# Optimization experiments

Hardware: AMD Instinct MI355X
Metric: run time of the kernel (lower is better)

## Reference

```python
import jax, jax.numpy as jnp
import numpy as np

N_NODES = 50000
N_EDGES = 800000
IN_DIM = 128
HID = 32
HEADS = 4
EMB = 64
NEG_SLOPE = 0.2
LN_EPS = 1e-5


def setup_inputs() -> dict:
    key = jax.random.key(0)
    ks = jax.random.split(key, 16)
    s = 0.1
    inp = {
        'x': jax.random.normal(ks[0], (N_NODES, IN_DIM), dtype=jnp.float32),
        'edge_index': jax.random.randint(ks[1], (2, N_EDGES), 0, N_NODES, dtype=jnp.int64),
        # GATConv 1: in=128 -> heads=4, out_per_head=32, concat -> 128
        'W1': jax.random.normal(ks[2], (IN_DIM, HEADS * HID), dtype=jnp.float32) * s,
        'att_src1': jax.random.normal(ks[3], (HEADS, HID), dtype=jnp.float32) * s,
        'att_dst1': jax.random.normal(ks[4], (HEADS, HID), dtype=jnp.float32) * s,
        'b1': jnp.zeros((HEADS * HID,), dtype=jnp.float32),
        'gamma1': jnp.ones((HEADS * HID,), dtype=jnp.float32),
        'beta1': jnp.zeros((HEADS * HID,), dtype=jnp.float32),
        # GATConv 2: in=128 -> heads=1, out=64, concat=False
        'W2': jax.random.normal(ks[5], (HEADS * HID, EMB), dtype=jnp.float32) * s,
        'att_src2': jax.random.normal(ks[6], (1, EMB), dtype=jnp.float32) * s,
        'att_dst2': jax.random.normal(ks[7], (1, EMB), dtype=jnp.float32) * s,
        'b2': jnp.zeros((EMB,), dtype=jnp.float32),
        'gamma2': jnp.ones((EMB,), dtype=jnp.float32),
        'beta2': jnp.zeros((EMB,), dtype=jnp.float32),
    }
    return inp


def _gat_conv(x, src, dst, W, att_src, att_dst):
    # x: [N, F_in]; src/dst: [E'] (self loops included); W: [F_in, H*C]
    N = x.shape[0]
    H, C = att_src.shape
    h = (x @ W).reshape(N, H, C)                          # [N, H, C]
    a_s = jnp.sum(h * att_src, axis=-1)                   # [N, H]
    a_d = jnp.sum(h * att_dst, axis=-1)                   # [N, H]
    e = jax.nn.leaky_relu(a_s[src] + a_d[dst], NEG_SLOPE) # [E', H]
    # segment softmax over destination-node neighborhoods
    m = jax.ops.segment_max(e, dst, num_segments=N)       # [N, H]
    ex = jnp.exp(e - m[dst])
    den = jax.ops.segment_sum(ex, dst, num_segments=N)    # [N, H]
    alpha = ex / den[dst]                                  # [E', H]
    msg = h[src] * alpha[:, :, None]                       # [E', H, C]
    return jax.ops.segment_sum(msg, dst, num_segments=N)  # [N, H, C]


def _layer_norm(x, gamma, beta):
    mu = jnp.mean(x, axis=-1, keepdims=True)
    var = jnp.var(x, axis=-1, keepdims=True)
    return (x - mu) * jax.lax.rsqrt(var + LN_EPS) * gamma + beta


def reference(x, edge_index, W1, att_src1, att_dst1, b1, gamma1, beta1,
              W2, att_src2, att_dst2, b2, gamma2, beta2):
    N = x.shape[0]
    loops = jnp.arange(N, dtype=edge_index.dtype)
    src = jnp.concatenate([edge_index[0], loops])  # PyG add_self_loops=True
    dst = jnp.concatenate([edge_index[1], loops])

    # gat1: heads=4, concat=True
    h1 = _gat_conv(x, src, dst, W1, att_src1, att_dst1)   # [N, 4, 32]
    h1 = h1.reshape(N, -1) + b1                            # [N, 128]
    h1 = jax.nn.relu(_layer_norm(h1, gamma1, beta1))
    # dropout is identity in eval mode

    # gat2: heads=1, concat=False (mean over the single head)
    h2 = _gat_conv(h1, src, dst, W2, att_src2, att_dst2)  # [N, 1, 64]
    h2 = h2.mean(axis=1) + b2                              # [N, 64]
    return _layer_norm(h2, gamma2, beta2)
```

## Files before the change

kernel.cpp:

```cpp
#include <hip/hip_runtime.h>
#include <hip/hip_bf16.h>
#include <math.h>

#define N_NODES 50000
#define N_EDGES 800000
#define HEADS 4
#define HID 32
#define D1 128
#define D2 64
#define NEG_SLOPE 0.2f
#define LN_EPS 1e-5f

#define NB_SCAN ((N_NODES + 255) / 256)
#define CAP 64
#define GB1 (((N_NODES + 127) / 128) * 2)
#define DEGB 784

__device__ __forceinline__ float lrelu(float x) { return x > 0.f ? x : NEG_SLOPE * x; }
__device__ __forceinline__ float bf2f(__hip_bfloat16 v) { return __bfloat162float(v); }

__global__ __launch_bounds__(256) void gemm1_att1_degree_kernel(
    const float* __restrict__ X, const float* __restrict__ W,
    __hip_bfloat16* __restrict__ Y,
    const float* __restrict__ att_src, const float* __restrict__ att_dst,
    float* __restrict__ a_s, float* __restrict__ a_d,
    const int* __restrict__ dst, int* __restrict__ deg, int* __restrict__ rank) {
    __shared__ float Wlds[128 * 64];
    if (blockIdx.x >= GB1) {
        int t0 = (blockIdx.x - GB1) * 256 + threadIdx.x;
        const int stride = DEGB * 256;
#pragma unroll
        for (int u = 0; u < 4; ++u) {
            int i = t0 + u * stride;
            if (i < N_EDGES) rank[i] = atomicAdd(&deg[dst[i]], 1);
        }
        return;
    }
    int tid = threadIdx.x;
    int rb = blockIdx.x >> 1;
    int half = blockIdx.x & 1;
    int cg = tid >> 6;
    int rg = tid & 63;
    int c0 = cg * 16;
    int gc0 = half * 64 + c0;
    int r0 = rb * 128 + rg * 2;

    for (int idx = tid; idx < 128 * 16; idx += 256) {
        int k = idx >> 4;
        int c4 = idx & 15;
        *(float4*)&Wlds[k * 64 + c4 * 4] =
            *(const float4*)&W[(size_t)k * 128 + half * 64 + c4 * 4];
    }
    __syncthreads();

    float acc[2][16];
#pragma unroll
    for (int i = 0; i < 2; ++i)
#pragma unroll
        for (int j = 0; j < 16; ++j) acc[i][j] = 0.f;

    const float* xrow[2];
#pragma unroll
    for (int i = 0; i < 2; ++i) {
        int ri = r0 + i;
        if (ri >= N_NODES) ri = N_NODES - 1;
        xrow[i] = X + (size_t)ri * 128;
    }

    for (int k = 0; k < 128; k += 4) {
        float4 xv[2];
#pragma unroll
        for (int i = 0; i < 2; ++i) xv[i] = *(const float4*)&xrow[i][k];
#pragma unroll
        for (int kk = 0; kk < 4; ++kk) {
            const float* wrow = &Wlds[(k + kk) * 64 + c0];
            const float4 w0 = *(const float4*)(wrow + 0);
            const float4 w1 = *(const float4*)(wrow + 4);
            const float4 w2 = *(const float4*)(wrow + 8);
            const float4 w3 = *(const float4*)(wrow + 12);
#pragma unroll
            for (int i = 0; i < 2; ++i) {
                float xk = (kk == 0) ? xv[i].x : (kk == 1) ? xv[i].y : (kk == 2) ? xv[i].z : xv[i].w;
                acc[i][0]  += xk * w0.x; acc[i][1]  += xk * w0.y;
                acc[i][2]  += xk * w0.z; acc[i][3]  += xk * w0.w;
                acc[i][4]  += xk * w1.x; acc[i][5]  += xk * w1.y;
                acc[i][6]  += xk * w1.z; acc[i][7]  += xk * w1.w;
                acc[i][8]  += xk * w2.x; acc[i][9]  += xk * w2.y;
                acc[i][10] += xk * w2.z; acc[i][11] += xk * w2.w;
                acc[i][12] += xk * w3.x; acc[i][13] += xk * w3.y;
                acc[i][14] += xk * w3.z; acc[i][15] += xk * w3.w;
            }
        }
    }

#pragma unroll
    for (int i = 0; i < 2; ++i) {
        int r = r0 + i;
        if (r < N_NODES) {
            __hip_bfloat162* yp = (__hip_bfloat162*)(Y + (size_t)r * 128 + gc0);
#pragma unroll
            for (int j = 0; j < 8; ++j) {
                __hip_bfloat162 p;
                p.x = __float2bfloat16(acc[i][2 * j]);
                p.y = __float2bfloat16(acc[i][2 * j + 1]);
                yp[j] = p;
            }
        }
    }

    int head = half * 2 + (cg >> 1);
    float asv[16], adv[16];
#pragma unroll
    for (int j = 0; j < 16; ++j) {
        asv[j] = att_src[head * 32 + (cg & 1) * 16 + j];
        adv[j] = att_dst[head * 32 + (cg & 1) * 16 + j];
    }
    float ps[2], pd[2];
#pragma unroll
    for (int i = 0; i < 2; ++i) {
        ps[i] = 0.f; pd[i] = 0.f;
#pragma unroll
        for (int j = 0; j < 16; ++j) {
            ps[i] += acc[i][j] * asv[j];
            pd[i] += acc[i][j] * adv[j];
        }
    }
    __syncthreads();
    float* red = Wlds;
#pragma unroll
    for (int i = 0; i < 2; ++i) {
        int rr = rg * 2 + i;
        red[rr * 4 + cg] = ps[i];
        red[512 + rr * 4 + cg] = pd[i];
    }
    __syncthreads();
    if (tid < 128) {
        int r = rb * 128 + tid;
        if (r < N_NODES) {
            float as0 = red[tid * 4 + 0] + red[tid * 4 + 1];
            float as1 = red[tid * 4 + 2] + red[tid * 4 + 3];
            float ad0 = red[512 + tid * 4 + 0] + red[512 + tid * 4 + 1];
            float ad1 = red[512 + tid * 4 + 2] + red[512 + tid * 4 + 3];
            a_s[r * 4 + half * 2 + 0] = as0;
            a_s[r * 4 + half * 2 + 1] = as1;
            a_d[r * 4 + half * 2 + 0] = ad0;
            a_d[r * 4 + half * 2 + 1] = ad1;
        }
    }
}

__global__ __launch_bounds__(256) void scan1_kernel(const int* __restrict__ deg,
                                                    int* __restrict__ rpl,
                                                    int* __restrict__ bsum) {
    int i = blockIdx.x * 256 + threadIdx.x;
    int v = (i < N_NODES) ? deg[i] : 0;
    int lane = threadIdx.x & 63;
    int w = threadIdx.x >> 6;
    int x = v;
#pragma unroll
    for (int off = 1; off < 64; off <<= 1) {
        int t = __shfl_up(x, off, 64);
        if (lane >= off) x += t;
    }
    __shared__ int wsum[4];
    if (lane == 63) wsum[w] = x;
    __syncthreads();
    int wo = 0;
    if (w > 0) wo += wsum[0];
    if (w > 1) wo += wsum[1];
    if (w > 2) wo += wsum[2];
    if (i <= N_NODES) rpl[i] = x - v + wo;
    if (threadIdx.x == 255) bsum[blockIdx.x] = x + wo;
}

__global__ __launch_bounds__(256) void scan2_kernel(const int* __restrict__ bsum,
                                                    int* __restrict__ boff) {
    int i = threadIdx.x;
    int v = (i < NB_SCAN) ? bsum[i] : 0;
    int lane = threadIdx.x & 63;
    int w = threadIdx.x >> 6;
    int x = v;
#pragma unroll
    for (int off = 1; off < 64; off <<= 1) {
        int t = __shfl_up(x, off, 64);
        if (lane >= off) x += t;
    }
    __shared__ int wsum[4];
    if (lane == 63) wsum[w] = x;
    __syncthreads();
    int wo = 0;
    if (w > 0) wo += wsum[0];
    if (w > 1) wo += wsum[1];
    if (w > 2) wo += wsum[2];
    if (i < NB_SCAN) boff[i] = x - v + wo;
}

__global__ __launch_bounds__(256) void scatter_kernel(const int* __restrict__ src,
                                                      const int* __restrict__ dst,
                                                      const int* __restrict__ rpl,
                                                      const int* __restrict__ boff,
                                                      const int* __restrict__ rank,
                                                      int* __restrict__ col) {
    int i = blockIdx.x * blockDim.x + threadIdx.x;
    if (i < N_EDGES) {
        int d = dst[i];
        int pos = rpl[d] + boff[d >> 8] + rank[i];
        col[pos] = src[i];
    }
}

__global__ __launch_bounds__(256) void agg1_kernel(const __hip_bfloat16* __restrict__ h,
                                                   const float* __restrict__ a_s,
                                                   const float* __restrict__ a_d,
                                                   const int* __restrict__ rpl,
                                                   const int* __restrict__ boff,
                                                   const int* __restrict__ col,
                                                   const float* __restrict__ b1,
                                                   const float* __restrict__ gamma,
                                                   const float* __restrict__ beta,
                                                   float* __restrict__ out) {
    __shared__ int colsh[4][CAP];
    __shared__ float wsh[4][CAP * 4];
    int wv = threadIdx.x >> 6;
    int lane = threadIdx.x & 63;
    int n = blockIdx.x * 4 + wv;
    int nn = (n < N_NODES) ? n : N_NODES - 1;
    int head = lane >> 4;
    int c = 2 * lane;

    const float4 ad4 = *(const float4*)&a_d[nn * 4];
    int beg = rpl[nn] + boff[nn >> 8];
    int end = rpl[nn + 1] + boff[(nn + 1) >> 8];
    int deg = end - beg;

    float den0 = 0.f, den1 = 0.f, den2 = 0.f, den3 = 0.f;
    for (int t = lane; t < deg; t += 64) {
        int s = col[beg + t];
        const float4 as4 = *(const float4*)&a_s[s * 4];
        float w0 = __expf(lrelu(as4.x + ad4.x));
        float w1 = __expf(lrelu(as4.y + ad4.y));
        float w2 = __expf(lrelu(as4.z + ad4.z));
        float w3 = __expf(lrelu(as4.w + ad4.w));
        if (t < CAP) {
            colsh[wv][t] = s;
            *(float4*)&wsh[wv][t * 4] = make_float4(w0, w1, w2, w3);
        }
        den0 += w0; den1 += w1; den2 += w2; den3 += w3;
    }
#pragma unroll
    for (int m = 1; m < 64; m <<= 1) {
        den0 += __shfl_xor(den0, m, 64);
        den1 += __shfl_xor(den1, m, 64);
        den2 += __shfl_xor(den2, m, 64);
        den3 += __shfl_xor(den3, m, 64);
    }
    float adh = (head == 0) ? ad4.x : (head == 1) ? ad4.y : (head == 2) ? ad4.z : ad4.w;
    float wself = __expf(lrelu(a_s[nn * 4 + head] + adh));
    float den = ((head == 0) ? den0 : (head == 1) ? den1 : (head == 2) ? den2 : den3) + wself;

    __syncthreads();

    float ax0 = 0.f, ay0 = 0.f, ax1 = 0.f, ay1 = 0.f;
    int m0 = (deg < CAP) ? deg : CAP;
    int j = 0;
    for (; j + 3 < m0; j += 4) {
        int s0 = colsh[wv][j + 0], s1 = colsh[wv][j + 1];
        int s2 = colsh[wv][j + 2], s3 = colsh[wv][j + 3];
        float w0 = wsh[wv][(j + 0) * 4 + head], w1 = wsh[wv][(j + 1) * 4 + head];
        float w2 = wsh[wv][(j + 2) * 4 + head], w3 = wsh[wv][(j + 3) * 4 + head];
        __hip_bfloat162 h0 = ((const __hip_bfloat162*)h)[(size_t)s0 * 64 + lane];
        __hip_bfloat162 h1 = ((const __hip_bfloat162*)h)[(size_t)s1 * 64 + lane];
        __hip_bfloat162 h2v = ((const __hip_bfloat162*)h)[(size_t)s2 * 64 + lane];
        __hip_bfloat162 h3 = ((const __hip_bfloat162*)h)[(size_t)s3 * 64 + lane];
        ax0 += w0 * bf2f(h0.x); ay0 += w0 * bf2f(h0.y);
        ax1 += w1 * bf2f(h1.x); ay1 += w1 * bf2f(h1.y);
        ax0 += w2 * bf2f(h2v.x); ay0 += w2 * bf2f(h2v.y);
        ax1 += w3 * bf2f(h3.x); ay1 += w3 * bf2f(h3.y);
    }
    for (; j < m0; ++j) {
        int s = colsh[wv][j];
        float w = wsh[wv][j * 4 + head];
        __hip_bfloat162 hv = ((const __hip_bfloat162*)h)[(size_t)s * 64 + lane];
        ax0 += w * bf2f(hv.x); ay0 += w * bf2f(hv.y);
    }
    for (; j < deg; ++j) {
        int s = col[beg + j];
        float w = __expf(lrelu(a_s[s * 4 + head] + adh));
        __hip_bfloat162 hv = ((const __hip_bfloat162*)h)[(size_t)s * 64 + lane];
        ax0 += w * bf2f(hv.x); ay0 += w * bf2f(hv.y);
    }
    {
        __hip_bfloat162 hv = ((const __hip_bfloat162*)h)[(size_t)nn * 64 + lane];
        ax0 += wself * bf2f(hv.x); ay0 += wself * bf2f(hv.y);
    }
    float inv = 1.f / den;
    float vx = (ax0 + ax1) * inv + b1[c];
    float vy = (ay0 + ay1) * inv + b1[c + 1];

    float s1 = vx + vy, s2 = vx * vx + vy * vy;
#pragma unroll
    for (int m = 1; m < 64; m <<= 1) {
        s1 += __shfl_xor(s1, m, 64);
        s2 += __shfl_xor(s2, m, 64);
    }
    float mean = s1 * (1.f / 128.f);
    float var = s2 * (1.f / 128.f) - mean * mean;
    float r = rsqrtf(var + LN_EPS);
    float ox = fmaxf(0.f, (vx - mean) * r * gamma[c] + beta[c]);
    float oy = fmaxf(0.f, (vy - mean) * r * gamma[c + 1] + beta[c + 1]);
    if (n < N_NODES) *(float2*)&out[(size_t)n * 128 + c] = make_float2(ox, oy);
}

__global__ __launch_bounds__(256) void gemm2_att2_kernel(const float* __restrict__ X,
                                                         const float* __restrict__ W,
                                                         __hip_bfloat16* __restrict__ Y,
                                                         const float* __restrict__ att_src,
                                                         const float* __restrict__ att_dst,
                                                         float* __restrict__ a_s,
                                                         float* __restrict__ a_d) {
    __shared__ float Wlds[128 * 64];
    int tid = threadIdx.x;
    int cg = tid >> 6;
    int rg = tid & 63;
    int c0 = cg * 16;
    int r0 = blockIdx.x * 128 + rg * 2;

    for (int idx = tid; idx < 128 * 16; idx += 256) {
        ((float4*)Wlds)[idx] = ((const float4*)W)[idx];
    }
    __syncthreads();

    float acc[2][16];
#pragma unroll
    for (int i = 0; i < 2; ++i)
#pragma unroll
        for (int j = 0; j < 16; ++j) acc[i][j] = 0.f;

    const float* xrow[2];
#pragma unroll
    for (int i = 0; i < 2; ++i) {
        int ri = r0 + i;
        if (ri >= N_NODES) ri = N_NODES - 1;
        xrow[i] = X + (size_t)ri * 128;
    }

    for (int k = 0; k < 128; k += 4) {
        float4 xv[2];
#pragma unroll
        for (int i = 0; i < 2; ++i) xv[i] = *(const float4*)&xrow[i][k];
#pragma unroll
        for (int kk = 0; kk < 4; ++kk) {
            const float* wrow = &Wlds[(k + kk) * 64 + c0];
            const float4 w0 = *(const float4*)(wrow + 0);
            const float4 w1 = *(const float4*)(wrow + 4);
            const float4 w2 = *(const float4*)(wrow + 8);
            const float4 w3 = *(const float4*)(wrow + 12);
#pragma unroll
            for (int i = 0; i < 2; ++i) {
                float xk = (kk == 0) ? xv[i].x : (kk == 1) ? xv[i].y : (kk == 2) ? xv[i].z : xv[i].w;
                acc[i][0]  += xk * w0.x; acc[i][1]  += xk * w0.y;
                acc[i][2]  += xk * w0.z; acc[i][3]  += xk * w0.w;
                acc[i][4]  += xk * w1.x; acc[i][5]  += xk * w1.y;
                acc[i][6]  += xk * w1.z; acc[i][7]  += xk * w1.w;
                acc[i][8]  += xk * w2.x; acc[i][9]  += xk * w2.y;
                acc[i][10] += xk * w2.z; acc[i][11] += xk * w2.w;
                acc[i][12] += xk * w3.x; acc[i][13] += xk * w3.y;
                acc[i][14] += xk * w3.z; acc[i][15] += xk * w3.w;
            }
        }
    }

#pragma unroll
    for (int i = 0; i < 2; ++i) {
        int r = r0 + i;
        if (r < N_NODES) {
            __hip_bfloat162* yp = (__hip_bfloat162*)(Y + (size_t)r * 64 + c0);
#pragma unroll
            for (int j = 0; j < 8; ++j) {
                __hip_bfloat162 p;
                p.x = __float2bfloat16(acc[i][2 * j]);
                p.y = __float2bfloat16(acc[i][2 * j + 1]);
                yp[j] = p;
            }
        }
    }

    float ps[2], pd[2];
#pragma unroll
    for (int i = 0; i < 2; ++i) {
        ps[i] = 0.f; pd[i] = 0.f;
#pragma unroll
        for (int j = 0; j < 16; ++j) {
            ps[i] += acc[i][j] * att_src[c0 + j];
            pd[i] += acc[i][j] * att_dst[c0 + j];
        }
    }
    __syncthreads();
    float* red = Wlds;
#pragma unroll
    for (int i = 0; i < 2; ++i) {
        int rr = rg * 2 + i;
        red[rr * 4 + cg] = ps[i];
        red[512 + rr * 4 + cg] = pd[i];
    }
    __syncthreads();
    if (tid < 128) {
        int r = blockIdx.x * 128 + tid;
        float as = red[tid * 4 + 0] + red[tid * 4 + 1] + red[tid * 4 + 2] + red[tid * 4 + 3];
        float ad = red[512 + tid * 4 + 0] + red[512 + tid * 4 + 1] +
                   red[512 + tid * 4 + 2] + red[512 + tid * 4 + 3];
        if (r < N_NODES) {
            a_s[r] = as;
            a_d[r] = ad;
        }
    }
}

__global__ __launch_bounds__(256) void agg2_kernel(const __hip_bfloat16* __restrict__ h,
                                                   const float* __restrict__ a_s,
                                                   const float* __restrict__ a_d,
                                                   const int* __restrict__ rpl,
                                                   const int* __restrict__ boff,
                                                   const int* __restrict__ col,
                                                   const float* __restrict__ b2,
                                                   const float* __restrict__ gamma,
                                                   const float* __restrict__ beta,
                                                   float* __restrict__ out) {
    __shared__ int colsh[4][CAP];
    __shared__ float wsh[4][CAP];
    int wv = threadIdx.x >> 6;
    int lane = threadIdx.x & 63;
    int n = blockIdx.x * 4 + wv;
    int nn = (n < N_NODES) ? n : N_NODES - 1;

    float adh = a_d[nn];
    int beg = rpl[nn] + boff[nn >> 8];
    int end = rpl[nn + 1] + boff[(nn + 1) >> 8];
    int deg = end - beg;

    float den = 0.f;
    for (int t = lane; t < deg; t += 64) {
        int s = col[beg + t];
        float w = __expf(lrelu(a_s[s] + adh));
        if (t < CAP) {
            colsh[wv][t] = s;
            wsh[wv][t] = w;
        }
        den += w;
    }
#pragma unroll
    for (int m = 1; m < 64; m <<= 1) den += __shfl_xor(den, m, 64);
    float wself = __expf(lrelu(a_s[nn] + adh));
    den += wself;

    __syncthreads();

    float a0 = 0.f, a1 = 0.f;
    int m0 = (deg < CAP) ? deg : CAP;
    int j = 0;
    for (; j + 3 < m0; j += 4) {
        int s0 = colsh[wv][j + 0], s1 = colsh[wv][j + 1];
        int s2 = colsh[wv][j + 2], s3 = colsh[wv][j + 3];
        float w0 = wsh[wv][j + 0], w1 = wsh[wv][j + 1];
        float w2 = wsh[wv][j + 2], w3 = wsh[wv][j + 3];
        a0 += w0 * bf2f(h[(size_t)s0 * 64 + lane]);
        a1 += w1 * bf2f(h[(size_t)s1 * 64 + lane]);
        a0 += w2 * bf2f(h[(size_t)s2 * 64 + lane]);
        a1 += w3 * bf2f(h[(size_t)s3 * 64 + lane]);
    }
    for (; j < m0; ++j) {
        a0 += wsh[wv][j] * bf2f(h[(size_t)colsh[wv][j] * 64 + lane]);
    }
    for (; j < deg; ++j) {
        int s = col[beg + j];
        float w = __expf(lrelu(a_s[s] + adh));
        a0 += w * bf2f(h[(size_t)s * 64 + lane]);
    }
    a0 += wself * bf2f(h[(size_t)nn * 64 + lane]);

    float v = (a0 + a1) / den + b2[lane];

    float s1 = v, s2 = v * v;
#pragma unroll
    for (int m = 1; m < 64; m <<= 1) {
        s1 += __shfl_xor(s1, m, 64);
        s2 += __shfl_xor(s2, m, 64);
    }
    float mean = s1 * (1.f / 64.f);
    float var = s2 * (1.f / 64.f) - mean * mean;
    float r = rsqrtf(var + LN_EPS);
    if (n < N_NODES) out[(size_t)n * 64 + lane] = (v - mean) * r * gamma[lane] + beta[lane];
}

extern "C" void kernel_launch(void* const* d_in, const int* in_sizes, int n_in,
                              void* d_out, int out_size, void* d_ws, size_t ws_size,
                              hipStream_t stream) {
    const float* x        = (const float*)d_in[0];
    const int*   ei       = (const int*)d_in[1];
    const float* W1       = (const float*)d_in[2];
    const float* att_src1 = (const float*)d_in[3];
    const float* att_dst1 = (const float*)d_in[4];
    const float* b1       = (const float*)d_in[5];
    const float* gamma1   = (const float*)d_in[6];
    const float* beta1    = (const float*)d_in[7];
    const float* W2       = (const float*)d_in[8];
    const float* att_src2 = (const float*)d_in[9];
    const float* att_dst2 = (const float*)d_in[10];
    const float* b2       = (const float*)d_in[11];
    const float* gamma2   = (const float*)d_in[12];
    const float* beta2    = (const float*)d_in[13];
    const int* src = ei;
    const int* dst = ei + N_EDGES;
    float* out = (float*)d_out;

    char* ws = (char*)d_ws;
    size_t off = 0;
    auto alloc = [&](size_t bytes) -> void* {
        void* p = ws + off;
        off += bytes;
        off = (off + 255) & ~(size_t)255;
        return p;
    };
    __hip_bfloat16* h1pre = (__hip_bfloat16*)alloc((size_t)N_NODES * 128 * 2);
    __hip_bfloat16* h2pre = (__hip_bfloat16*)alloc((size_t)N_NODES * 64 * 2);
    float* a_s1   = (float*)alloc((size_t)N_NODES * 4 * 4);
    float* a_d1   = (float*)alloc((size_t)N_NODES * 4 * 4);
    float* h1n    = (float*)alloc((size_t)N_NODES * 128 * 4);
    float* a_s2   = (float*)alloc((size_t)N_NODES * 4);
    float* a_d2   = (float*)alloc((size_t)N_NODES * 4);
    int* deg      = (int*)alloc((size_t)N_NODES * 4);
    int* rpl      = (int*)alloc((size_t)(N_NODES + 1) * 4);
    int* col      = (int*)alloc((size_t)N_EDGES * 4);
    int* rank     = (int*)alloc((size_t)N_EDGES * 4);
    int* bsum     = (int*)alloc((size_t)NB_SCAN * 4);
    int* boff     = (int*)alloc((size_t)NB_SCAN * 4);

    hipMemsetAsync(deg, 0, (size_t)N_NODES * 4, stream);

    const int EB = (N_EDGES + 255) / 256;
    const int NWB = (N_NODES + 3) / 4;

    gemm1_att1_degree_kernel<<<GB1 + DEGB, 256, 0, stream>>>(
        x, W1, h1pre, att_src1, att_dst1, a_s1, a_d1, dst, deg, rank);
    scan1_kernel<<<NB_SCAN, 256, 0, stream>>>(deg, rpl, bsum);
    scan2_kernel<<<1, 256, 0, stream>>>(bsum, boff);
    scatter_kernel<<<EB, 256, 0, stream>>>(src, dst, rpl, boff, rank, col);

    agg1_kernel<<<NWB, 256, 0, stream>>>(h1pre, a_s1, a_d1, rpl, boff, col, b1, gamma1, beta1, h1n);

    gemm2_att2_kernel<<<(N_NODES + 127) / 128, 256, 0, stream>>>(
        h1n, W2, h2pre, att_src2, att_dst2, a_s2, a_d2);
    agg2_kernel<<<NWB, 256, 0, stream>>>(h2pre, a_s2, a_d2, rpl, boff, col, b2, gamma2, beta2, out);
}
```

Before: 261.9 us.

## Stage X tiles transposed in LDS and use 4x8 register tiles in both GEMMs

Both node-feature GEMM kernels now load 32-wide K slices of X cooperatively into a transposed, padded LDS tile rather than having each thread read its own rows straight from global memory. Each thread computes a 4-row by 8-column tile, and the attention-score partial sums are reduced with a cross-half-wave shuffle before a smaller LDS reduction. The aim is coalesced X loads and fewer redundant global reads per block. In exchange it adds extra barriers per K-block and more LDS use, which may lower occupancy.

```diff
diff --git a/kernel.cpp b/kernel.cpp
--- a/kernel.cpp
+++ b/kernel.cpp
@@ -26,6 +26,7 @@
     float* __restrict__ a_s, float* __restrict__ a_d,
     const int* __restrict__ dst, int* __restrict__ deg, int* __restrict__ rank) {
     __shared__ float Wlds[128 * 64];
+    __shared__ float Xlds[32][132];
     if (blockIdx.x >= GB1) {
         int t0 = (blockIdx.x - GB1) * 256 + threadIdx.x;
         const int stride = DEGB * 256;
@@ -39,67 +40,64 @@
     int tid = threadIdx.x;
     int rb = blockIdx.x >> 1;
     int half = blockIdx.x & 1;
-    int cg = tid >> 6;
-    int rg = tid & 63;
-    int c0 = cg * 16;
+    int wv = tid >> 6;
+    int lane = tid & 63;
+    int rl = lane & 31;
+    int ch = lane >> 5;
+    int c0 = wv * 16 + ch * 8;
     int gc0 = half * 64 + c0;
-    int r0 = rb * 128 + rg * 2;
+    int r0 = rb * 128;
+    int rowbase = rl * 4;
 
     for (int idx = tid; idx < 128 * 16; idx += 256) {
-        int k = idx >> 4;
-        int c4 = idx & 15;
+        int k = idx >> 4, c4 = idx & 15;
         *(float4*)&Wlds[k * 64 + c4 * 4] =
             *(const float4*)&W[(size_t)k * 128 + half * 64 + c4 * 4];
     }
-    __syncthreads();
-
-    float acc[2][16];
-#pragma unroll
-    for (int i = 0; i < 2; ++i)
-#pragma unroll
-        for (int j = 0; j < 16; ++j) acc[i][j] = 0.f;
-
-    const float* xrow[2];
-#pragma unroll
-    for (int i = 0; i < 2; ++i) {
-        int ri = r0 + i;
-        if (ri >= N_NODES) ri = N_NODES - 1;
-        xrow[i] = X + (size_t)ri * 128;
-    }
-
-    for (int k = 0; k < 128; k += 4) {
-        float4 xv[2];
-#pragma unroll
-        for (int i = 0; i < 2; ++i) xv[i] = *(const float4*)&xrow[i][k];
-#pragma unroll
-        for (int kk = 0; kk < 4; ++kk) {
-            const float* wrow = &Wlds[(k + kk) * 64 + c0];
+
+    float acc[4][8];
+#pragma unroll
+    for (int i = 0; i < 4; ++i)
+#pragma unroll
+        for (int j = 0; j < 8; ++j) acc[i][j] = 0.f;
+
+    for (int kb = 0; kb < 128; kb += 32) {
+        __syncthreads();
+        for (int i = tid; i < 1024; i += 256) {
+            int row = i >> 3;
+            int kq = i & 7;
+            int rr = r0 + row; if (rr >= N_NODES) rr = N_NODES - 1;
+            float4 v = *(const float4*)&X[(size_t)rr * 128 + kb + kq * 4];
+            Xlds[kq * 4 + 0][row] = v.x;
+            Xlds[kq * 4 + 1][row] = v.y;
+            Xlds[kq * 4 + 2][row] = v.z;
+            Xlds[kq * 4 + 3][row] = v.w;
+        }
+        __syncthreads();
+#pragma unroll 8
+        for (int k = 0; k < 32; ++k) {
+            float4 xv = *(const float4*)&Xlds[k][rowbase];
+            const float* wrow = &Wlds[(kb + k) * 64 + c0];
             const float4 w0 = *(const float4*)(wrow + 0);
             const float4 w1 = *(const float4*)(wrow + 4);
-            const float4 w2 = *(const float4*)(wrow + 8);
-            const float4 w3 = *(const float4*)(wrow + 12);
-#pragma unroll
-            for (int i = 0; i < 2; ++i) {
-                float xk = (kk == 0) ? xv[i].x : (kk == 1) ? xv[i].y : (kk == 2) ? xv[i].z : xv[i].w;
-                acc[i][0]  += xk * w0.x; acc[i][1]  += xk * w0.y;
-                acc[i][2]  += xk * w0.z; acc[i][3]  += xk * w0.w;
-                acc[i][4]  += xk * w1.x; acc[i][5]  += xk * w1.y;
-                acc[i][6]  += xk * w1.z; acc[i][7]  += xk * w1.w;
-                acc[i][8]  += xk * w2.x; acc[i][9]  += xk * w2.y;
-                acc[i][10] += xk * w2.z; acc[i][11] += xk * w2.w;
-                acc[i][12] += xk * w3.x; acc[i][13] += xk * w3.y;
-                acc[i][14] += xk * w3.z; acc[i][15] += xk * w3.w;
+#pragma unroll
+            for (int i = 0; i < 4; ++i) {
+                float xk = (i == 0) ? xv.x : (i == 1) ? xv.y : (i == 2) ? xv.z : xv.w;
+                acc[i][0] += xk * w0.x; acc[i][1] += xk * w0.y;
+                acc[i][2] += xk * w0.z; acc[i][3] += xk * w0.w;
+                acc[i][4] += xk * w1.x; acc[i][5] += xk * w1.y;
+                acc[i][6] += xk * w1.z; acc[i][7] += xk * w1.w;
             }
         }
     }
 
 #pragma unroll
-    for (int i = 0; i < 2; ++i) {
-        int r = r0 + i;
+    for (int i = 0; i < 4; ++i) {
+        int r = r0 + rowbase + i;
         if (r < N_NODES) {
             __hip_bfloat162* yp = (__hip_bfloat162*)(Y + (size_t)r * 128 + gc0);
 #pragma unroll
-            for (int j = 0; j < 8; ++j) {
+            for (int j = 0; j < 4; ++j) {
                 __hip_bfloat162 p;
                 p.x = __float2bfloat16(acc[i][2 * j]);
                 p.y = __float2bfloat16(acc[i][2 * j + 1]);
@@ -108,39 +106,35 @@
         }
     }
 
-    int head = half * 2 + (cg >> 1);
-    float asv[16], adv[16];
-#pragma unroll
-    for (int j = 0; j < 16; ++j) {
-        asv[j] = att_src[head * 32 + (cg & 1) * 16 + j];
-        adv[j] = att_dst[head * 32 + (cg & 1) * 16 + j];
-    }
-    float ps[2], pd[2];
-#pragma unroll
-    for (int i = 0; i < 2; ++i) {
+    float ps[4], pd[4];
+#pragma unroll
+    for (int i = 0; i < 4; ++i) {
         ps[i] = 0.f; pd[i] = 0.f;
 #pragma unroll
-        for (int j = 0; j < 16; ++j) {
-            ps[i] += acc[i][j] * asv[j];
-            pd[i] += acc[i][j] * adv[j];
-        }
-    }
-    __syncthreads();
-    float* red = Wlds;
-#pragma unroll
-    for (int i = 0; i < 2; ++i) {
-        int rr = rg * 2 + i;
-        red[rr * 4 + cg] = ps[i];
-        red[512 + rr * 4 + cg] = pd[i];
+        for (int j = 0; j < 8; ++j) {
+            ps[i] += acc[i][j] * att_src[gc0 + j];
+            pd[i] += acc[i][j] * att_dst[gc0 + j];
+        }
+        ps[i] += __shfl_xor(ps[i], 32, 64);
+        pd[i] += __shfl_xor(pd[i], 32, 64);
+    }
+    __syncthreads();
+    float* red = &Xlds[0][0];
+    if (ch == 0) {
+#pragma unroll
+        for (int i = 0; i < 4; ++i) {
+            red[wv * 128 + rowbase + i] = ps[i];
+            red[512 + wv * 128 + rowbase + i] = pd[i];
+        }
     }
     __syncthreads();
     if (tid < 128) {
-        int r = rb * 128 + tid;
+        int r = r0 + tid;
         if (r < N_NODES) {
-            float as0 = red[tid * 4 + 0] + red[tid * 4 + 1];
-            float as1 = red[tid * 4 + 2] + red[tid * 4 + 3];
-            float ad0 = red[512 + tid * 4 + 0] + red[512 + tid * 4 + 1];
-            float ad1 = red[512 + tid * 4 + 2] + red[512 + tid * 4 + 3];
+            float as0 = red[tid] + red[128 + tid];
+            float as1 = red[256 + tid] + red[384 + tid];
+            float ad0 = red[512 + tid] + red[640 + tid];
+            float ad1 = red[768 + tid] + red[896 + tid];
             a_s[r * 4 + half * 2 + 0] = as0;
             a_s[r * 4 + half * 2 + 1] = as1;
             a_d[r * 4 + half * 2 + 0] = ad0;
@@ -319,64 +313,62 @@
                                                          float* __restrict__ a_s,
                                                          float* __restrict__ a_d) {
     __shared__ float Wlds[128 * 64];
+    __shared__ float Xlds[32][132];
     int tid = threadIdx.x;
-    int cg = tid >> 6;
-    int rg = tid & 63;
-    int c0 = cg * 16;
-    int r0 = blockIdx.x * 128 + rg * 2;
-
-    for (int idx = tid; idx < 128 * 16; idx += 256) {
+    int wv = tid >> 6;
+    int lane = tid & 63;
+    int rl = lane & 31;
+    int ch = lane >> 5;
+    int c0 = wv * 16 + ch * 8;
+    int r0 = blockIdx.x * 128;
+    int rowbase = rl * 4;
+
+    for (int idx = tid; idx < 128 * 16; idx += 256)
         ((float4*)Wlds)[idx] = ((const float4*)W)[idx];
-    }
-    __syncthreads();
-
-    float acc[2][16];
-#pragma unroll
-    for (int i = 0; i < 2; ++i)
-#pragma unroll
-        for (int j = 0; j < 16; ++j) acc[i][j] = 0.f;
-
-    const float* xrow[2];
-#pragma unroll
-    for (int i = 0; i < 2; ++i) {
-        int ri = r0 + i;
-        if (ri >= N_NODES) ri = N_NODES - 1;
-        xrow[i] = X + (size_t)ri * 128;
-    }
-
-    for (int k = 0; k < 128; k += 4) {
-        float4 xv[2];
-#pragma unroll
-        for (int i = 0; i < 2; ++i) xv[i] = *(const float4*)&xrow[i][k];
-#pragma unroll
-        for (int kk = 0; kk < 4; ++kk) {
-            const float* wrow = &Wlds[(k + kk) * 64 + c0];
+
+    float acc[4][8];
+#pragma unroll
+    for (int i = 0; i < 4; ++i)
+#pragma unroll
+        for (int j = 0; j < 8; ++j) acc[i][j] = 0.f;
+
+    for (int kb = 0; kb < 128; kb += 32) {
+        __syncthreads();
+        for (int i = tid; i < 1024; i += 256) {
+            int row = i >> 3;
+            int kq = i & 7;
+            int rr = r0 + row; if (rr >= N_NODES) rr = N_NODES - 1;
+            float4 v = *(const float4*)&X[(size_t)rr * 128 + kb + kq * 4];
+            Xlds[kq * 4 + 0][row] = v.x;
+            Xlds[kq * 4 + 1][row] = v.y;
+            Xlds[kq * 4 + 2][row] = v.z;
+            Xlds[kq * 4 + 3][row] = v.w;
+        }
+        __syncthreads();
+#pragma unroll 8
+        for (int k = 0; k < 32; ++k) {
+            float4 xv = *(const float4*)&Xlds[k][rowbase];
+            const float* wrow = &Wlds[(kb + k) * 64 + c0];
             const float4 w0 = *(const float4*)(wrow + 0);
             const float4 w1 = *(const float4*)(wrow + 4);
-            const float4 w2 = *(const float4*)(wrow + 8);
-            const float4 w3 = *(const float4*)(wrow + 12);
-#pragma unroll
-            for (int i = 0; i < 2; ++i) {
-                float xk = (kk == 0) ? xv[i].x : (kk == 1) ? xv[i].y : (kk == 2) ? xv[i].z : xv[i].w;
-                acc[i][0]  += xk * w0.x; acc[i][1]  += xk * w0.y;
-                acc[i][2]  += xk * w0.z; acc[i][3]  += xk * w0.w;
-                acc[i][4]  += xk * w1.x; acc[i][5]  += xk * w1.y;
-                acc[i][6]  += xk * w1.z; acc[i][7]  += xk * w1.w;
-                acc[i][8]  += xk * w2.x; acc[i][9]  += xk * w2.y;
-                acc[i][10] += xk * w2.z; acc[i][11] += xk * w2.w;
-                acc[i][12] += xk * w3.x; acc[i][13] += xk * w3.y;
-                acc[i][14] += xk * w3.z; acc[i][15] += xk * w3.w;
+#pragma unroll
+            for (int i = 0; i < 4; ++i) {
+                float xk = (i == 0) ? xv.x : (i == 1) ? xv.y : (i == 2) ? xv.z : xv.w;
+                acc[i][0] += xk * w0.x; acc[i][1] += xk * w0.y;
+                acc[i][2] += xk * w0.z; acc[i][3] += xk * w0.w;
+                acc[i][4] += xk * w1.x; acc[i][5] += xk * w1.y;
+                acc[i][6] += xk * w1.z; acc[i][7] += xk * w1.w;
             }
         }
     }
 
 #pragma unroll
-    for (int i = 0; i < 2; ++i) {
-        int r = r0 + i;
+    for (int i = 0; i < 4; ++i) {
+        int r = r0 + rowbase + i;
         if (r < N_NODES) {
             __hip_bfloat162* yp = (__hip_bfloat162*)(Y + (size_t)r * 64 + c0);
 #pragma unroll
-            for (int j = 0; j < 8; ++j) {
+            for (int j = 0; j < 4; ++j) {
                 __hip_bfloat162 p;
                 p.x = __float2bfloat16(acc[i][2 * j]);
                 p.y = __float2bfloat16(acc[i][2 * j + 1]);
@@ -385,31 +377,33 @@
         }
     }
 
-    float ps[2], pd[2];
-#pragma unroll
-    for (int i = 0; i < 2; ++i) {
+    float ps[4], pd[4];
+#pragma unroll
+    for (int i = 0; i < 4; ++i) {
         ps[i] = 0.f; pd[i] = 0.f;
 #pragma unroll
-        for (int j = 0; j < 16; ++j) {
+        for (int j = 0; j < 8; ++j) {
             ps[i] += acc[i][j] * att_src[c0 + j];
             pd[i] += acc[i][j] * att_dst[c0 + j];
         }
-    }
-    __syncthreads();
-    float* red = Wlds;
-#pragma unroll
-    for (int i = 0; i < 2; ++i) {
-        int rr = rg * 2 + i;
-        red[rr * 4 + cg] = ps[i];
-        red[512 + rr * 4 + cg] = pd[i];
+        ps[i] += __shfl_xor(ps[i], 32, 64);
+        pd[i] += __shfl_xor(pd[i], 32, 64);
+    }
+    __syncthreads();
+    float* red = &Xlds[0][0];
+    if (ch == 0) {
+#pragma unroll
+        for (int i = 0; i < 4; ++i) {
+            red[wv * 128 + rowbase + i] = ps[i];
+            red[512 + wv * 128 + rowbase + i] = pd[i];
+        }
     }
     __syncthreads();
     if (tid < 128) {
-        int r = blockIdx.x * 128 + tid;
-        float as = red[tid * 4 + 0] + red[tid * 4 + 1] + red[tid * 4 + 2] + red[tid * 4 + 3];
-        float ad = red[512 + tid * 4 + 0] + red[512 + tid * 4 + 1] +
-                   red[512 + tid * 4 + 2] + red[512 + tid * 4 + 3];
+        int r = r0 + tid;
         if (r < N_NODES) {
+            float as = red[tid] + red[128 + tid] + red[256 + tid] + red[384 + tid];
+            float ad = red[512 + tid] + red[640 + tid] + red[768 + tid] + red[896 + tid];
             a_s[r] = as;
             a_d[r] = ad;
         }
```

New measurement: 266.9 us. Within noise of the previous version (+1.9%).
